# Kernel tuning notes

Measured on AMD Instinct MI355X. Metric: run time of the kernel, lower is better.

Reference implementation:

```python
import jax, jax.numpy as jnp
import numpy as np
import math

B, C, MAPS, HEADS, F, W = 2, 8, 4, 8, 256, 1024
HD = F // HEADS  # head dim = 32


def conv2d(x, w, b):
    # x [B,Ci,H,W], w [Co,Ci,3,3], SAME padding 1
    y = jax.lax.conv_general_dilated(x, w, (1, 1), [(1, 1), (1, 1)],
                                     dimension_numbers=('NCHW', 'OIHW', 'NCHW'))
    return y + b[None, :, None, None]


def mcl_feat(x, w):
    # MultichannelLinear feature transform: per-channel linear over feature dim
    # x [B,C,Fin,W], w [C,Fout,Fin] -> [B,C,Fout,W]
    return jnp.einsum('bcfw,cgf->bcgw', x, w)


def rope(x):
    # lucidrains-style rotary embedding over seq dim (-2); x [..., S, D]
    d = x.shape[-1]
    s = x.shape[-2]
    inv = 1.0 / (10000.0 ** (jnp.arange(0, d, 2, dtype=jnp.float32) / d))
    fr = jnp.arange(s, dtype=jnp.float32)[:, None] * inv[None, :]  # [S, D/2]
    cos = jnp.repeat(jnp.cos(fr), 2, axis=-1).astype(x.dtype)  # [S, D]
    sin = jnp.repeat(jnp.sin(fr), 2, axis=-1).astype(x.dtype)
    x2 = x.reshape(*x.shape[:-1], d // 2, 2)
    xr = jnp.stack((-x2[..., 1], x2[..., 0]), axis=-1).reshape(x.shape)
    return x * cos + xr * sin


def setup_inputs() -> dict:
    key = jax.random.key(0)
    ks = jax.random.split(key, 16)
    p = lambda k, shp, s=0.02: (jax.random.normal(k, shp, dtype=jnp.float32) * s)
    inp = {
        'x': jax.random.normal(ks[0], (B, C, F, W), dtype=jnp.float32),
        'prev_qk': jax.random.normal(ks[1], (B, MAPS, HEADS, W, W), dtype=jnp.float32),
        'wq_conv': p(ks[2], (MAPS, C, 3, 3)), 'bq_conv': jnp.zeros((MAPS,), jnp.float32),
        'wq_lin': p(ks[3], (MAPS, F, F)),
        'wk_conv': p(ks[4], (MAPS, C, 3, 3)), 'bk_conv': jnp.zeros((MAPS,), jnp.float32),
        'wk_lin': p(ks[5], (MAPS, F, F)),
        'wv_conv': p(ks[6], (MAPS, C, 3, 3)), 'bv_conv': jnp.zeros((MAPS,), jnp.float32),
        'wv_lin': p(ks[7], (MAPS, F, F)),
        'wo_pw': p(ks[8], (C + MAPS, F, F)),
        'wo_dw': p(ks[9], (C, C + MAPS)),
    }
    return inp


def reference(x, prev_qk, wq_conv, bq_conv, wq_lin, wk_conv, bk_conv, wk_lin,
              wv_conv, bv_conv, wv_lin, wo_pw, wo_dw):
    b, c, h, w = x.shape

    def proj(w_conv, b_conv, w_lin):
        y = mcl_feat(conv2d(x, w_conv, b_conv), w_lin)  # [B,M,F,W]
        # transpose(2,3) -> [B,M,W,F] -> split heads -> [B,M,Hd,W? ] permute
        y = y.transpose(0, 1, 3, 2).reshape(b, MAPS, w, HEADS, HD)
        return y.transpose(0, 1, 3, 2, 4)  # [B,M,Heads,W,HD]

    q = rope(proj(wq_conv, bq_conv, wq_lin))
    k = rope(proj(wk_conv, bk_conv, wk_lin))
    v = proj(wv_conv, bv_conv, wv_lin)

    # NOTE: scale is sqrt(h) = sqrt(feature/height dim), as in the original code
    qk = jnp.einsum('bmnqd,bmnkd->bmnqk', q, k) / math.sqrt(h)
    qk = qk + prev_qk
    a = jnp.einsum('bmnqk,bmnkd->bmnqd', jax.nn.softmax(qk, axis=-1), v)
    # [B,M,Heads,W,HD] -> [B,M,W,Heads*HD] -> [B,M,F,W]
    a = a.transpose(0, 1, 3, 2, 4).reshape(b, MAPS, w, -1).transpose(0, 1, 3, 2)

    cat = jnp.concatenate((x, a), axis=1)  # [B, C+M, F, W]
    out = jnp.einsum('bcfw,oc->bofw', mcl_feat(cat, wo_pw), wo_dw)  # o_proj
    return out, qk
```

## Files before the change

kernel.cpp:

```cpp
#include <hip/hip_runtime.h>
#include <hip/hip_bf16.h>
#include <stdint.h>


typedef __attribute__((ext_vector_type(8))) short s16x8;
typedef __attribute__((ext_vector_type(4))) float f32x4;

#define MFMA16(a, b, c) __builtin_amdgcn_mfma_f32_16x16x32_bf16((a), (b), (c), 0, 0, 0)

__device__ __forceinline__ short f2bf(float f) {
  unsigned u = __builtin_bit_cast(unsigned, f);
  u = (u + 0x7FFFu + ((u >> 16) & 1u)) >> 16;
  return (short)u;
}
__device__ __forceinline__ unsigned pack2(float a, float b) {
  return (unsigned)(unsigned short)f2bf(a) | ((unsigned)(unsigned short)f2bf(b) << 16);
}
__device__ __forceinline__ float bf2f(unsigned u) {
  return __builtin_bit_cast(float, u << 16);
}

__global__ __launch_bounds__(256) void k_prep(const float* wq, const float* wk,
                                              const float* wv, const float* wo,
                                              short* wlin, short* wob, float* ct, float* st) {
  int i = blockIdx.x * 256 + threadIdx.x;
  if (i < 262144) wlin[i] = f2bf(wq[i]);
  else if (i < 524288) wlin[i] = f2bf(wk[i - 262144]);
  else if (i < 786432) wlin[i] = f2bf(wv[i - 524288]);
  if (i < 786432) wob[i] = f2bf(wo[i]);
  if (i < 16384) {
    int w = i >> 4, j = i & 15;
    float inv = exp2f(-(float)j * (13.287712379549449f / 16.0f));
    float ang = (float)w * inv;
    ct[i] = cosf(ang);
    st[i] = sinf(ang);
  }
}

__device__ __forceinline__ void loadrow(float* r, const float* xc, int f, int w0) {
  if (f < 0 || f > 255) {
#pragma unroll
    for (int jj = 0; jj < 6; ++jj) r[jj] = 0.f;
    return;
  }
  const float* row = xc + f * 1024;
#pragma unroll
  for (int jj = 0; jj < 6; ++jj) {
    int wc = w0 - 1 + jj;
    r[jj] = (wc >= 0 && wc < 1024) ? row[wc] : 0.f;
  }
}

__global__ __launch_bounds__(256) void k_conv(const float* x, const float* wqc, const float* bq,
                                              const float* wkc, const float* bk,
                                              const float* wvc, const float* bv, short* y) {
  int blk = blockIdx.x;
  int m_ = blk >> 7;
  int b_ = (blk >> 6) & 1;
  int fs = blk & 63;
  int f0 = fs * 4;
  int w0 = threadIdx.x * 4;
  const float* xb = x + (size_t)b_ * 2097152;
  const float* wp_[3] = {wqc + m_ * 72, wkc + m_ * 72, wvc + m_ * 72};
  float bias_[3] = {bq[m_], bk[m_], bv[m_]};

  float acc[3][4][4];
#pragma unroll
  for (int p = 0; p < 3; ++p)
#pragma unroll
    for (int fi = 0; fi < 4; ++fi)
#pragma unroll
      for (int j = 0; j < 4; ++j) acc[p][fi][j] = bias_[p];

  for (int c = 0; c < 8; ++c) {
    const float* xc = xb + c * 262144;
    float w9[3][9];
#pragma unroll
    for (int p = 0; p < 3; ++p)
#pragma unroll
      for (int t = 0; t < 9; ++t) w9[p][t] = wp_[p][c * 9 + t];
    float rows[6][6];
#pragma unroll
    for (int ri = 0; ri < 6; ++ri) loadrow(rows[ri], xc, f0 - 1 + ri, w0);
#pragma unroll
    for (int fi = 0; fi < 4; ++fi) {
#pragma unroll
      for (int p = 0; p < 3; ++p) {
#pragma unroll
        for (int j = 0; j < 4; ++j) {
          float s = acc[p][fi][j];
          s += rows[fi][j] * w9[p][0] + rows[fi][j + 1] * w9[p][1] + rows[fi][j + 2] * w9[p][2];
          s += rows[fi + 1][j] * w9[p][3] + rows[fi + 1][j + 1] * w9[p][4] + rows[fi + 1][j + 2] * w9[p][5];
          s += rows[fi + 2][j] * w9[p][6] + rows[fi + 2][j + 1] * w9[p][7] + rows[fi + 2][j + 2] * w9[p][8];
          acc[p][fi][j] = s;
        }
      }
    }
  }
#pragma unroll
  for (int p = 0; p < 3; ++p) {
    int mat = p * 8 + b_ * 4 + m_;
    short* yp = y + (size_t)mat * 262144;
#pragma unroll
    for (int fi = 0; fi < 4; ++fi) {
      uint2 pk;
      pk.x = pack2(acc[p][fi][0], acc[p][fi][1]);
      pk.y = pack2(acc[p][fi][2], acc[p][fi][3]);
      *(uint2*)(yp + (f0 + fi) * 1024 + w0) = pk;
    }
  }
}

__global__ __launch_bounds__(256) void k_ty(const short* y, short* yT) {
  __shared__ short tile[64][66];
  int blk = blockIdx.x;
  int mat = blk >> 6;
  int t = blk & 63;
  int f0 = (t >> 4) * 64, w0 = (t & 15) * 64;
  int j = threadIdx.x & 63, i0 = threadIdx.x >> 6;
  const short* sp = y + (size_t)mat * 262144 + f0 * 1024 + w0;
#pragma unroll
  for (int k = 0; k < 16; ++k) {
    int i = i0 + k * 4;
    tile[j][i] = sp[i * 1024 + j];
  }
  __syncthreads();
  short* dp = yT + (size_t)mat * 262144 + w0 * 256 + f0;
#pragma unroll
  for (int k = 0; k < 16; ++k) {
    int i = i0 + k * 4;
    dp[i * 256 + j] = tile[i][j];
  }
}

__global__ __launch_bounds__(256) void k_tx(const float* x, short* xT) {
  __shared__ short tile[64][66];
  int blk = blockIdx.x;
  int mat = blk >> 6;
  int t = blk & 63;
  int f0 = (t >> 4) * 64, w0 = (t & 15) * 64;
  int j = threadIdx.x & 63, i0 = threadIdx.x >> 6;
  const float* sp = x + (size_t)mat * 262144 + f0 * 1024 + w0;
#pragma unroll
  for (int k = 0; k < 16; ++k) {
    int i = i0 + k * 4;
    tile[j][i] = f2bf(sp[i * 1024 + j]);
  }
  __syncthreads();
  short* dp = xT + (size_t)mat * 262144 + w0 * 256 + f0;
#pragma unroll
  for (int k = 0; k < 16; ++k) {
    int i = i0 + k * 4;
    dp[i * 256 + j] = tile[i][j];
  }
}

__global__ __launch_bounds__(256) void k_qkv(const short* wlin, const short* yT,
                                             const float* ct, const float* st,
                                             short* qws, short* kws, short* vws) {
  int blk = blockIdx.x;
  int pbm = blk >> 4, wt = blk & 15;
  int p = pbm >> 3, bm = pbm & 7;
  int m_ = bm & 3;
  int tid = threadIdx.x, wv = tid >> 6, l = tid & 63, lr = l & 15, lg = l >> 4;
  const short* wl = wlin + (p * 4 + m_) * 65536;
  const short* yp = yT + (size_t)pbm * 262144;
  int w0 = wt * 64;
  int G0 = wv * 64;
  f32x4 acc[4][4];
#pragma unroll
  for (int i = 0; i < 4; ++i)
#pragma unroll
    for (int j = 0; j < 4; ++j) acc[i][j] = (f32x4){0.f, 0.f, 0.f, 0.f};

  if (p < 2) {
    for (int kc = 0; kc < 256; kc += 32) {
      s16x8 A[4], Bf[4];
#pragma unroll
      for (int gs = 0; gs < 4; ++gs)
        A[gs] = *(const s16x8*)(wl + (G0 + gs * 16 + lr) * 256 + kc + lg * 8);
#pragma unroll
      for (int s = 0; s < 4; ++s)
        Bf[s] = *(const s16x8*)(yp + (w0 + s * 16 + lr) * 256 + kc + lg * 8);
#pragma unroll
      for (int gs = 0; gs < 4; ++gs)
#pragma unroll
        for (int s = 0; s < 4; ++s) acc[gs][s] = MFMA16(A[gs], Bf[s], acc[gs][s]);
    }
    short* dst = (p == 0) ? qws : kws;
    float scale = (p == 0) ? 0.0625f : 1.0f;
#pragma unroll
    for (int gs = 0; gs < 4; ++gs) {
      int g0v = G0 + gs * 16 + lg * 4;
      int h = g0v >> 5, d0 = g0v & 31;
      int i0 = d0 >> 1;
#pragma unroll
      for (int s = 0; s < 4; ++s) {
        int w = w0 + s * 16 + lr;
        float c0 = ct[w * 16 + i0], sn0 = st[w * 16 + i0];
        float c1 = ct[w * 16 + i0 + 1], sn1 = st[w * 16 + i0 + 1];
        f32x4 v = acc[gs][s];
        float e0 = (v[0] * c0 - v[1] * sn0) * scale;
        float e1 = (v[1] * c0 + v[0] * sn0) * scale;
        float e2 = (v[2] * c1 - v[3] * sn1) * scale;
        float e3 = (v[3] * c1 + v[2] * sn1) * scale;
        uint2 pk;
        pk.x = pack2(e0, e1);
        pk.y = pack2(e2, e3);
        *(uint2*)(dst + (((size_t)bm * 8 + h) * 1024 + w) * 32 + d0) = pk;
      }
    }
  } else {
    for (int kc = 0; kc < 256; kc += 32) {
      s16x8 A[4], Bf[4];
#pragma unroll
      for (int s = 0; s < 4; ++s)
        A[s] = *(const s16x8*)(yp + (w0 + s * 16 + lr) * 256 + kc + lg * 8);
#pragma unroll
      for (int gs = 0; gs < 4; ++gs)
        Bf[gs] = *(const s16x8*)(wl + (G0 + gs * 16 + lr) * 256 + kc + lg * 8);
#pragma unroll
      for (int s = 0; s < 4; ++s)
#pragma unroll
        for (int gs = 0; gs < 4; ++gs) acc[s][gs] = MFMA16(A[s], Bf[gs], acc[s][gs]);
    }
#pragma unroll
    for (int s = 0; s < 4; ++s) {
      int wb = w0 + s * 16 + lg * 4;
#pragma unroll
      for (int gs = 0; gs < 4; ++gs) {
        int g = G0 + gs * 16 + lr;
        f32x4 v = acc[s][gs];
        uint2 pk;
        pk.x = pack2(v[0], v[1]);
        pk.y = pack2(v[2], v[3]);
        *(uint2*)(vws + ((size_t)bm * 256 + g) * 1024 + wb) = pk;
      }
    }
  }
}

__device__ __forceinline__ void attn_tile(int t, int tn, f32x4 (&pc)[4], f32x4 (&pn)[4],
                                          const float* pptr, float* qoptr,
                                          const short* kp, const short* vp,
                                          const s16x8& qf, char* Sb, char* Pb,
                                          int lr, int lg, f32x4& o0, f32x4& o1, f32x4& ps) {
#pragma unroll
  for (int j = 0; j < 4; ++j)
    pn[j] = *(const f32x4*)(pptr + j * 4096 + tn * 64);
  int k0 = t * 64;
  s16x8 kf[4];
#pragma unroll
  for (int s = 0; s < 4; ++s)
    kf[s] = *(const s16x8*)(kp + (k0 + s * 16 + lr) * 32 + lg * 8);
  const f32x4 z4 = {0.f, 0.f, 0.f, 0.f};
#pragma unroll
  for (int s = 0; s < 4; ++s) {
    f32x4 Sx = MFMA16(kf[s], qf, z4);
    *(f32x4*)(Sb + lr * 256 + ((s * 64 + lg * 16) ^ ((lr & 7) << 4))) = Sx;
  }
#pragma unroll
  for (int j = 0; j < 4; ++j) {
    int r = j * 4 + lg;
    f32x4 rv = *(const f32x4*)(Sb + r * 256 + ((lr * 16) ^ ((r & 7) << 4)));
    rv += pc[j];
    __builtin_nontemporal_store(rv, (f32x4*)(qoptr + j * 4096 + t * 64));
    float e0 = __expf(rv[0]), e1 = __expf(rv[1]);
    float e2 = __expf(rv[2]), e3 = __expf(rv[3]);
    ps[j] += (e0 + e1) + (e2 + e3);
    uint2 pk;
    pk.x = pack2(e0, e1);
    pk.y = pack2(e2, e3);
    *(uint2*)(Pb + r * 128 + ((lr * 8) ^ ((r & 7) << 4))) = pk;
  }
#pragma unroll
  for (int kc = 0; kc < 2; ++kc) {
    s16x8 pa = *(const s16x8*)(Pb + lr * 128 + ((kc * 64 + lg * 16) ^ ((lr & 7) << 4)));
    s16x8 vf0 = *(const s16x8*)(vp + lr * 1024 + k0 + kc * 32 + lg * 8);
    o0 = MFMA16(pa, vf0, o0);
    s16x8 vf1 = *(const s16x8*)(vp + (16 + lr) * 1024 + k0 + kc * 32 + lg * 8);
    o1 = MFMA16(pa, vf1, o1);
  }
}

__global__ __launch_bounds__(256, 4) void k_attn(const short* qws, const short* kws,
                                                 const short* vws, const float* prev,
                                                 float* qko, short* aT) {
  int blk = blockIdx.x;
  int bmh = blk >> 4;
  int h = bmh & 7;
  int bm = bmh >> 3;
  int tid = threadIdx.x;
  int wv = tid >> 6, l = tid & 63, lr = l & 15, lg = l >> 4;
  int qt = (blk & 15) * 4 + wv;
  int q0 = qt * 16;
  const short* qp = qws + (size_t)bmh * 32768;
  const short* kp = kws + (size_t)bmh * 32768;
  const short* vp = vws + ((size_t)bm * 256 + h * 32) * 1024;
  const float* pptr = prev + (size_t)bmh * 1048576 + (size_t)(q0 + lg) * 1024 + lr * 4;
  float* qoptr = qko + (size_t)bmh * 1048576 + (size_t)(q0 + lg) * 1024 + lr * 4;

  __shared__ float s_s[4][16][64];
  __shared__ short s_p[4][16][64];
  char* Sb = (char*)&s_s[wv][0][0];
  char* Pb = (char*)&s_p[wv][0][0];

  s16x8 qf = *(const s16x8*)(qp + (q0 + lr) * 32 + lg * 8);
  f32x4 o0 = {0.f, 0.f, 0.f, 0.f}, o1 = {0.f, 0.f, 0.f, 0.f};
  f32x4 ps = {0.f, 0.f, 0.f, 0.f};

  f32x4 pA[4], pB[4];
#pragma unroll
  for (int j = 0; j < 4; ++j) pA[j] = *(const f32x4*)(pptr + j * 4096);

  for (int t = 0; t < 16; t += 2) {
    attn_tile(t, t + 1, pA, pB, pptr, qoptr, kp, vp, qf, Sb, Pb, lr, lg, o0, o1, ps);
    attn_tile(t + 1, (t + 2 < 16) ? t + 2 : 15, pB, pA, pptr, qoptr, kp, vp, qf, Sb, Pb, lr, lg, o0, o1, ps);
  }

#pragma unroll
  for (int j = 0; j < 4; ++j) {
    float s = ps[j];
    s += __shfl_xor(s, 1);
    s += __shfl_xor(s, 2);
    s += __shfl_xor(s, 4);
    s += __shfl_xor(s, 8);
    ps[j] = s;
  }
  if (lr == 0) {
#pragma unroll
    for (int j = 0; j < 4; ++j) *(float*)(Sb + (j * 4 + lg) * 4) = ps[j];
  }
  f32x4 sums = *(const f32x4*)(Sb + lg * 16);
  f32x4 inv = {1.f / sums[0], 1.f / sums[1], 1.f / sums[2], 1.f / sums[3]};
  o0 *= inv;
  o1 *= inv;
  short* ap = aT + (size_t)bm * 262144;
#pragma unroll
  for (int r = 0; r < 4; ++r) {
    int row = q0 + lg * 4 + r;
    ap[row * 256 + h * 32 + lr] = f2bf(o0[r]);
    ap[row * 256 + h * 32 + 16 + lr] = f2bf(o1[r]);
  }
}

__global__ __launch_bounds__(256) void k_zproj(const short* wopw, const short* xT,
                                               const short* aT, short* z) {
  int blk = blockIdx.x;
  int bc = blk >> 4, wt = blk & 15;
  int b_ = bc / 12, c_ = bc % 12;
  const short* src = (c_ < 8) ? (xT + ((size_t)b_ * 8 + c_) * 262144)
                              : (aT + ((size_t)b_ * 4 + (c_ - 8)) * 262144);
  const short* wl = wopw + c_ * 65536;
  int tid = threadIdx.x, wv = tid >> 6, l = tid & 63, lr = l & 15, lg = l >> 4;
  int w0 = wt * 64, G0 = wv * 64;
  f32x4 acc[4][4];
#pragma unroll
  for (int i = 0; i < 4; ++i)
#pragma unroll
    for (int j = 0; j < 4; ++j) acc[i][j] = (f32x4){0.f, 0.f, 0.f, 0.f};
  for (int kc = 0; kc < 256; kc += 32) {
    s16x8 A[4], Bf[4];
#pragma unroll
    for (int s = 0; s < 4; ++s)
      A[s] = *(const s16x8*)(src + (w0 + s * 16 + lr) * 256 + kc + lg * 8);
#pragma unroll
    for (int gs = 0; gs < 4; ++gs)
      Bf[gs] = *(const s16x8*)(wl + (G0 + gs * 16 + lr) * 256 + kc + lg * 8);
#pragma unroll
    for (int s = 0; s < 4; ++s)
#pragma unroll
      for (int gs = 0; gs < 4; ++gs) acc[s][gs] = MFMA16(A[s], Bf[gs], acc[s][gs]);
  }
  short* zp = z + (size_t)bc * 262144;
#pragma unroll
  for (int s = 0; s < 4; ++s) {
    int wb = w0 + s * 16 + lg * 4;
#pragma unroll
    for (int gs = 0; gs < 4; ++gs) {
      int g = G0 + gs * 16 + lr;
      f32x4 v = acc[s][gs];
      uint2 pk;
      pk.x = pack2(v[0], v[1]);
      pk.y = pack2(v[2], v[3]);
      *(uint2*)(zp + g * 1024 + wb) = pk;
    }
  }
}

__global__ __launch_bounds__(256) void k_dw(const short* z, const float* dw, float* out0) {
  __shared__ float wdw[96];
  if (threadIdx.x < 96) wdw[threadIdx.x] = dw[threadIdx.x];
  __syncthreads();
  int id = blockIdx.x * 256 + threadIdx.x;
  int w4 = id & 255, g = (id >> 8) & 255, b_ = id >> 16;
  const short* zb = z + ((size_t)b_ * 12) * 262144 + g * 1024 + w4 * 4;
  float zv[12][4];
#pragma unroll
  for (int c = 0; c < 12; ++c) {
    uint2 u = *(const uint2*)(zb + (size_t)c * 262144);
    zv[c][0] = bf2f(u.x & 0xffffu);
    zv[c][1] = bf2f(u.x >> 16);
    zv[c][2] = bf2f(u.y & 0xffffu);
    zv[c][3] = bf2f(u.y >> 16);
  }
  float* ob = out0 + ((size_t)b_ * 8) * 262144 + g * 1024 + w4 * 4;
#pragma unroll
  for (int o = 0; o < 8; ++o) {
    f32x4 s = {0.f, 0.f, 0.f, 0.f};
#pragma unroll
    for (int c = 0; c < 12; ++c) {
      float wc = wdw[o * 12 + c];
      s[0] += wc * zv[c][0];
      s[1] += wc * zv[c][1];
      s[2] += wc * zv[c][2];
      s[3] += wc * zv[c][3];
    }
    __builtin_nontemporal_store(s, (f32x4*)(ob + (size_t)o * 262144));
  }
}

extern "C" void kernel_launch(void* const* d_in, const int* in_sizes, int n_in,
                              void* d_out, int out_size, void* d_ws, size_t ws_size,
                              hipStream_t stream) {
  const float* x = (const float*)d_in[0];
  const float* prevqk = (const float*)d_in[1];
  const float* wq_conv = (const float*)d_in[2];
  const float* bq = (const float*)d_in[3];
  const float* wq_lin = (const float*)d_in[4];
  const float* wk_conv = (const float*)d_in[5];
  const float* bk = (const float*)d_in[6];
  const float* wk_lin = (const float*)d_in[7];
  const float* wv_conv = (const float*)d_in[8];
  const float* bv = (const float*)d_in[9];
  const float* wv_lin = (const float*)d_in[10];
  const float* wo_pw = (const float*)d_in[11];
  const float* wo_dw = (const float*)d_in[12];

  float* out0 = (float*)d_out;
  float* qkout = out0 + 4194304;

  char* ws = (char*)d_ws;
  short* wlin_b = (short*)ws;
  short* wopw_b = wlin_b + 786432;
  float* ct = (float*)(ws + 3145728);
  float* st = ct + 16384;
  short* y_b = (short*)(ws + 3276800);
  short* yT_b = y_b + 6291456;
  short* q_b = yT_b + 6291456;
  short* k_b = q_b + 2097152;
  short* v_b = k_b + 2097152;
  short* xT_b = v_b + 2097152;
  short* aT_b = xT_b + 4194304;
  short* z_b = (short*)(ws + 53608448);

  k_prep<<<3072, 256, 0, stream>>>(wq_lin, wk_lin, wv_lin, wo_pw, wlin_b, wopw_b, ct, st);
  k_conv<<<512, 256, 0, stream>>>(x, wq_conv, bq, wk_conv, bk, wv_conv, bv, y_b);
  k_ty<<<1536, 256, 0, stream>>>(y_b, yT_b);
  k_tx<<<1024, 256, 0, stream>>>(x, xT_b);
  k_qkv<<<384, 256, 0, stream>>>(wlin_b, yT_b, ct, st, q_b, k_b, v_b);
  k_attn<<<1024, 256, 0, stream>>>(q_b, k_b, v_b, prevqk, qkout, aT_b);
  k_zproj<<<384, 256, 0, stream>>>(wopw_b, xT_b, aT_b, z_b);
  k_dw<<<512, 256, 0, stream>>>(z_b, wo_dw, out0);
}
```

Measured before the change: 241.6 us.

## Restructure attention into single-wave blocks with 256-key windows and row-contiguous prev_qk access

Each block of the attention kernel becomes a single 64-lane wave that owns 16 query rows, and keys are processed in 256-wide windows. The score tile is staged through 16KB of shared memory so each lane reads and writes contiguous 16-byte chunks along a full 1024-float row of prev_qk and the qk output, instead of the earlier 64-float strips. This is meant to improve coalescing of the dominant fp32 prev_qk read and qk write, and to issue 16 row loads per window for more memory-level parallelism. In exchange it uses more registers and shared memory per wave, gives up the previous double-buffered prefetch, and adds a shared-memory reduction for the row sums.

```diff
diff --git a/kernel.cpp b/kernel.cpp
--- a/kernel.cpp
+++ b/kernel.cpp
@@ -240,98 +240,91 @@
   }
 }
 
-__device__ __forceinline__ void attn_tile(int t, int tn, f32x4 (&pc)[4], f32x4 (&pn)[4],
-                                          const float* pptr, float* qoptr,
-                                          const short* kp, const short* vp,
-                                          const s16x8& qf, char* Sb, char* Pb,
-                                          int lr, int lg, f32x4& o0, f32x4& o1, f32x4& ps) {
-#pragma unroll
-  for (int j = 0; j < 4; ++j)
-    pn[j] = *(const f32x4*)(pptr + j * 4096 + tn * 64);
-  int k0 = t * 64;
-  s16x8 kf[4];
-#pragma unroll
-  for (int s = 0; s < 4; ++s)
-    kf[s] = *(const s16x8*)(kp + (k0 + s * 16 + lr) * 32 + lg * 8);
-  const f32x4 z4 = {0.f, 0.f, 0.f, 0.f};
-#pragma unroll
-  for (int s = 0; s < 4; ++s) {
-    f32x4 Sx = MFMA16(kf[s], qf, z4);
-    *(f32x4*)(Sb + lr * 256 + ((s * 64 + lg * 16) ^ ((lr & 7) << 4))) = Sx;
-  }
-#pragma unroll
-  for (int j = 0; j < 4; ++j) {
-    int r = j * 4 + lg;
-    f32x4 rv = *(const f32x4*)(Sb + r * 256 + ((lr * 16) ^ ((r & 7) << 4)));
-    rv += pc[j];
-    __builtin_nontemporal_store(rv, (f32x4*)(qoptr + j * 4096 + t * 64));
-    float e0 = __expf(rv[0]), e1 = __expf(rv[1]);
-    float e2 = __expf(rv[2]), e3 = __expf(rv[3]);
-    ps[j] += (e0 + e1) + (e2 + e3);
-    uint2 pk;
-    pk.x = pack2(e0, e1);
-    pk.y = pack2(e2, e3);
-    *(uint2*)(Pb + r * 128 + ((lr * 8) ^ ((r & 7) << 4))) = pk;
-  }
-#pragma unroll
-  for (int kc = 0; kc < 2; ++kc) {
-    s16x8 pa = *(const s16x8*)(Pb + lr * 128 + ((kc * 64 + lg * 16) ^ ((lr & 7) << 4)));
-    s16x8 vf0 = *(const s16x8*)(vp + lr * 1024 + k0 + kc * 32 + lg * 8);
-    o0 = MFMA16(pa, vf0, o0);
-    s16x8 vf1 = *(const s16x8*)(vp + (16 + lr) * 1024 + k0 + kc * 32 + lg * 8);
-    o1 = MFMA16(pa, vf1, o1);
-  }
-}
-
-__global__ __launch_bounds__(256, 4) void k_attn(const short* qws, const short* kws,
-                                                 const short* vws, const float* prev,
-                                                 float* qko, short* aT) {
-  int blk = blockIdx.x;
-  int bmh = blk >> 4;
+__global__ __launch_bounds__(64, 2) void k_attn(const short* qws, const short* kws,
+                                                const short* vws, const float* prev,
+                                                float* qko, short* aT) {
+  int blk = blockIdx.x;
+  int bmh = blk >> 6;
+  int qt = blk & 63;
   int h = bmh & 7;
   int bm = bmh >> 3;
-  int tid = threadIdx.x;
-  int wv = tid >> 6, l = tid & 63, lr = l & 15, lg = l >> 4;
-  int qt = (blk & 15) * 4 + wv;
+  int l = threadIdx.x;
+  int lr = l & 15, lg = l >> 4;
   int q0 = qt * 16;
   const short* qp = qws + (size_t)bmh * 32768;
   const short* kp = kws + (size_t)bmh * 32768;
   const short* vp = vws + ((size_t)bm * 256 + h * 32) * 1024;
-  const float* pptr = prev + (size_t)bmh * 1048576 + (size_t)(q0 + lg) * 1024 + lr * 4;
-  float* qoptr = qko + (size_t)bmh * 1048576 + (size_t)(q0 + lg) * 1024 + lr * 4;
-
-  __shared__ float s_s[4][16][64];
-  __shared__ short s_p[4][16][64];
-  char* Sb = (char*)&s_s[wv][0][0];
-  char* Pb = (char*)&s_p[wv][0][0];
+  const float* pvb = prev + (size_t)bmh * 1048576 + (size_t)q0 * 1024 + l * 4;
+  float* qob = qko + (size_t)bmh * 1048576 + (size_t)q0 * 1024 + l * 4;
+
+  __shared__ char smem[16384];
+  int swl = (l & 7) << 4;
 
   s16x8 qf = *(const s16x8*)(qp + (q0 + lr) * 32 + lg * 8);
   f32x4 o0 = {0.f, 0.f, 0.f, 0.f}, o1 = {0.f, 0.f, 0.f, 0.f};
-  f32x4 ps = {0.f, 0.f, 0.f, 0.f};
-
-  f32x4 pA[4], pB[4];
-#pragma unroll
-  for (int j = 0; j < 4; ++j) pA[j] = *(const f32x4*)(pptr + j * 4096);
-
-  for (int t = 0; t < 16; t += 2) {
-    attn_tile(t, t + 1, pA, pB, pptr, qoptr, kp, vp, qf, Sb, Pb, lr, lg, o0, o1, ps);
-    attn_tile(t + 1, (t + 2 < 16) ? t + 2 : 15, pB, pA, pptr, qoptr, kp, vp, qf, Sb, Pb, lr, lg, o0, o1, ps);
-  }
-
-#pragma unroll
-  for (int j = 0; j < 4; ++j) {
-    float s = ps[j];
-    s += __shfl_xor(s, 1);
-    s += __shfl_xor(s, 2);
-    s += __shfl_xor(s, 4);
-    s += __shfl_xor(s, 8);
-    ps[j] = s;
-  }
-  if (lr == 0) {
-#pragma unroll
-    for (int j = 0; j < 4; ++j) *(float*)(Sb + (j * 4 + lg) * 4) = ps[j];
-  }
-  f32x4 sums = *(const f32x4*)(Sb + lg * 16);
+  float rs[16];
+#pragma unroll
+  for (int r = 0; r < 16; ++r) rs[r] = 0.f;
+  const f32x4 z4 = {0.f, 0.f, 0.f, 0.f};
+  int swlr = (lr & 7) << 4;
+
+  for (int win = 0; win < 4; ++win) {
+    int kw = win * 256;
+    f32x4 pr[16];
+#pragma unroll
+    for (int r = 0; r < 16; ++r) pr[r] = *(const f32x4*)(pvb + (size_t)r * 1024 + kw);
+
+#pragma unroll
+    for (int t = 0; t < 4; ++t) {
+      s16x8 kf[4];
+#pragma unroll
+      for (int s = 0; s < 4; ++s)
+        kf[s] = *(const s16x8*)(kp + (kw + t * 64 + s * 16 + lr) * 32 + lg * 8);
+#pragma unroll
+      for (int s = 0; s < 4; ++s) {
+        f32x4 Sx = MFMA16(kf[s], qf, z4);
+        *(f32x4*)(smem + lr * 1024 + ((t * 256 + s * 64 + lg * 16) ^ swlr)) = Sx;
+      }
+    }
+
+#pragma unroll
+    for (int r = 0; r < 16; ++r) {
+      f32x4 sv = *(const f32x4*)(smem + r * 1024 + ((l * 16) ^ ((r & 7) << 4)));
+      f32x4 v = sv + pr[r];
+      __builtin_nontemporal_store(v, (f32x4*)(qob + (size_t)r * 1024 + kw));
+      float e0 = __expf(v[0]), e1 = __expf(v[1]);
+      float e2 = __expf(v[2]), e3 = __expf(v[3]);
+      rs[r] += (e0 + e1) + (e2 + e3);
+      uint2 pk;
+      pk.x = pack2(e0, e1);
+      pk.y = pack2(e2, e3);
+      *(uint2*)(smem + r * 512 + ((l * 8) ^ ((r & 7) << 4))) = pk;
+    }
+
+#pragma unroll
+    for (int t = 0; t < 4; ++t) {
+#pragma unroll
+      for (int kc = 0; kc < 2; ++kc) {
+        s16x8 pa = *(const s16x8*)(smem + lr * 512 + ((t * 128 + kc * 64 + lg * 16) ^ swlr));
+        s16x8 vf0 = *(const s16x8*)(vp + lr * 1024 + kw + t * 64 + kc * 32 + lg * 8);
+        o0 = MFMA16(pa, vf0, o0);
+        s16x8 vf1 = *(const s16x8*)(vp + (16 + lr) * 1024 + kw + t * 64 + kc * 32 + lg * 8);
+        o1 = MFMA16(pa, vf1, o1);
+      }
+    }
+  }
+
+  float* sred = (float*)smem;
+#pragma unroll
+  for (int r = 0; r < 16; ++r) sred[r * 64 + l] = rs[r];
+  int rj = l >> 2, c0 = (l & 3) * 16;
+  float tsum = 0.f;
+#pragma unroll
+  for (int j = 0; j < 16; ++j) tsum += sred[rj * 64 + c0 + j];
+  tsum += __shfl_xor(tsum, 1);
+  tsum += __shfl_xor(tsum, 2);
+  if ((l & 3) == 0) *(float*)(smem + 8192 + rj * 4) = tsum;
+  f32x4 sums = *(const f32x4*)(smem + 8192 + lg * 16);
   f32x4 inv = {1.f / sums[0], 1.f / sums[1], 1.f / sums[2], 1.f / sums[3]};
   o0 *= inv;
   o1 *= inv;
@@ -459,7 +452,7 @@
   k_ty<<<1536, 256, 0, stream>>>(y_b, yT_b);
   k_tx<<<1024, 256, 0, stream>>>(x, xT_b);
   k_qkv<<<384, 256, 0, stream>>>(wlin_b, yT_b, ct, st, q_b, k_b, v_b);
-  k_attn<<<1024, 256, 0, stream>>>(q_b, k_b, v_b, prevqk, qkout, aT_b);
+  k_attn<<<4096, 64, 0, stream>>>(q_b, k_b, v_b, prevqk, qkout, aT_b);
   k_zproj<<<384, 256, 0, stream>>>(wopw_b, xT_b, aT_b, z_b);
   k_dw<<<512, 256, 0, stream>>>(z_b, wo_dw, out0);
 }
```

New measurement: 243.3 us. Within noise of the previous version (+0.7%).

## Stage full K and V for a head in LDS and deepen prev_qk prefetch

Applied to the files above, without the earlier changes.

The attention kernel now copies the whole K (1024x32) and V (32x1024) slice for its head into a large swizzled shared-memory buffer once per block, then reads K and V fragments from LDS instead of global memory. The prev_qk prefetch is moved two windows ahead, issued after the P stores. The aim is to cut repeated global or L2 traffic for K/V and hide prev_qk latency. The ~152KB of LDS and launch_bounds(256,1) limit occupancy to one block per CU, which reduces latency hiding on what is mostly a memory-bound stream of prev_qk and qk.

```diff
diff --git a/kernel.cpp b/kernel.cpp
--- a/kernel.cpp
+++ b/kernel.cpp
@@ -240,96 +240,114 @@
   }
 }
 
-__device__ __forceinline__ void attn_tile(int t, int tn, f32x4 (&pc)[4], f32x4 (&pn)[4],
-                                          const float* pptr, float* qoptr,
-                                          const short* kp, const short* vp,
-                                          const s16x8& qf, char* Sb, char* Pb,
-                                          int lr, int lg, f32x4& o0, f32x4& o1, f32x4& ps) {
-#pragma unroll
-  for (int j = 0; j < 4; ++j)
-    pn[j] = *(const f32x4*)(pptr + j * 4096 + tn * 64);
-  int k0 = t * 64;
-  s16x8 kf[4];
-#pragma unroll
-  for (int s = 0; s < 4; ++s)
-    kf[s] = *(const s16x8*)(kp + (k0 + s * 16 + lr) * 32 + lg * 8);
-  const f32x4 z4 = {0.f, 0.f, 0.f, 0.f};
-#pragma unroll
-  for (int s = 0; s < 4; ++s) {
-    f32x4 Sx = MFMA16(kf[s], qf, z4);
-    *(f32x4*)(Sb + lr * 256 + ((s * 64 + lg * 16) ^ ((lr & 7) << 4))) = Sx;
-  }
-#pragma unroll
-  for (int j = 0; j < 4; ++j) {
-    int r = j * 4 + lg;
-    f32x4 rv = *(const f32x4*)(Sb + r * 256 + ((lr * 16) ^ ((r & 7) << 4)));
-    rv += pc[j];
-    __builtin_nontemporal_store(rv, (f32x4*)(qoptr + j * 4096 + t * 64));
-    float e0 = __expf(rv[0]), e1 = __expf(rv[1]);
-    float e2 = __expf(rv[2]), e3 = __expf(rv[3]);
-    ps[j] += (e0 + e1) + (e2 + e3);
-    uint2 pk;
-    pk.x = pack2(e0, e1);
-    pk.y = pack2(e2, e3);
-    *(uint2*)(Pb + r * 128 + ((lr * 8) ^ ((r & 7) << 4))) = pk;
-  }
-#pragma unroll
-  for (int kc = 0; kc < 2; ++kc) {
-    s16x8 pa = *(const s16x8*)(Pb + lr * 128 + ((kc * 64 + lg * 16) ^ ((lr & 7) << 4)));
-    s16x8 vf0 = *(const s16x8*)(vp + lr * 1024 + k0 + kc * 32 + lg * 8);
-    o0 = MFMA16(pa, vf0, o0);
-    s16x8 vf1 = *(const s16x8*)(vp + (16 + lr) * 1024 + k0 + kc * 32 + lg * 8);
-    o1 = MFMA16(pa, vf1, o1);
-  }
-}
-
-__global__ __launch_bounds__(256, 4) void k_attn(const short* qws, const short* kws,
+__global__ __launch_bounds__(256, 1) void k_attn(const short* qws, const short* kws,
                                                  const short* vws, const float* prev,
                                                  float* qko, short* aT) {
+  __shared__ char smem[155648];
   int blk = blockIdx.x;
   int bmh = blk >> 4;
-  int h = bmh & 7;
-  int bm = bmh >> 3;
+  int qg = blk & 15;
+  int h = bmh & 7, bm = bmh >> 3;
   int tid = threadIdx.x;
   int wv = tid >> 6, l = tid & 63, lr = l & 15, lg = l >> 4;
-  int qt = (blk & 15) * 4 + wv;
-  int q0 = qt * 16;
-  const short* qp = qws + (size_t)bmh * 32768;
   const short* kp = kws + (size_t)bmh * 32768;
   const short* vp = vws + ((size_t)bm * 256 + h * 32) * 1024;
-  const float* pptr = prev + (size_t)bmh * 1048576 + (size_t)(q0 + lg) * 1024 + lr * 4;
-  float* qoptr = qko + (size_t)bmh * 1048576 + (size_t)(q0 + lg) * 1024 + lr * 4;
-
-  __shared__ float s_s[4][16][64];
-  __shared__ short s_p[4][16][64];
-  char* Sb = (char*)&s_s[wv][0][0];
-  char* Pb = (char*)&s_p[wv][0][0];
-
+
+  {
+    int row4 = tid >> 2, c = tid & 3;
+#pragma unroll
+    for (int i = 0; i < 16; ++i) {
+      int row = i * 64 + row4;
+      s16x8 kv = *(const s16x8*)(kp + row * 32 + c * 8);
+      *(s16x8*)(smem + row * 64 + ((c * 16) ^ ((row & 3) << 4))) = kv;
+    }
+    int g2 = tid >> 7, cb = (tid & 127) * 16;
+#pragma unroll
+    for (int i = 0; i < 16; ++i) {
+      int g = i * 2 + g2;
+      s16x8 vv = *(const s16x8*)(vp + g * 1024 + (cb >> 1));
+      *(s16x8*)(smem + 65536 + g * 2048 + (cb ^ ((g & 7) << 4))) = vv;
+    }
+  }
+  __syncthreads();
+
+  int q0 = qg * 64 + wv * 16;
+  const short* qp = qws + (size_t)bmh * 32768;
   s16x8 qf = *(const s16x8*)(qp + (q0 + lr) * 32 + lg * 8);
+  char* Sb = smem + 131072 + wv * 4096;
+  char* Pb = smem + 147456 + wv * 2048;
+  const float* pvb = prev + (size_t)bmh * 1048576 + (size_t)q0 * 1024;
+  float* qob = qko + (size_t)bmh * 1048576 + (size_t)q0 * 1024;
+  int pcol = (l & 15) * 4;
+  int pcolb = pcol * 4;
   f32x4 o0 = {0.f, 0.f, 0.f, 0.f}, o1 = {0.f, 0.f, 0.f, 0.f};
-  f32x4 ps = {0.f, 0.f, 0.f, 0.f};
+  f32x4 rs = {0.f, 0.f, 0.f, 0.f};
+  const f32x4 z4 = {0.f, 0.f, 0.f, 0.f};
+
+  auto attn_win = [&](int w, f32x4(&pr)[4]) {
+    int k0 = w * 64;
+#pragma unroll
+    for (int s = 0; s < 4; ++s) {
+      int krow = k0 + s * 16 + lr;
+      s16x8 kf = *(const s16x8*)(smem + krow * 64 + ((lg * 16) ^ ((krow & 3) << 4)));
+      f32x4 sx = MFMA16(kf, qf, z4);
+      *(f32x4*)(Sb + lr * 256 + ((s * 64 + lg * 16) ^ ((lr & 7) << 4))) = sx;
+    }
+#pragma unroll
+    for (int j = 0; j < 4; ++j) {
+      int qr = j * 4 + lg;
+      f32x4 sv = *(const f32x4*)(Sb + qr * 256 + (pcolb ^ ((qr & 7) << 4)));
+      f32x4 v = sv + pr[j];
+      __builtin_nontemporal_store(v, (f32x4*)(qob + (size_t)qr * 1024 + k0 + pcol));
+      float e0 = __expf(v[0]), e1 = __expf(v[1]);
+      float e2 = __expf(v[2]), e3 = __expf(v[3]);
+      rs[j] += (e0 + e1) + (e2 + e3);
+      uint2 pk;
+      pk.x = pack2(e0, e1);
+      pk.y = pack2(e2, e3);
+      *(uint2*)(Pb + qr * 128 + (((l & 15) * 8) ^ ((qr & 7) << 4))) = pk;
+    }
+    if (w + 2 < 16) {
+#pragma unroll
+      for (int j = 0; j < 4; ++j)
+        pr[j] = *(const f32x4*)(pvb + (size_t)(j * 4 + lg) * 1024 + (w + 2) * 64 + pcol);
+    }
+#pragma unroll
+    for (int kc = 0; kc < 2; ++kc) {
+      s16x8 pa = *(const s16x8*)(Pb + lr * 128 + ((kc * 64 + lg * 16) ^ ((lr & 7) << 4)));
+      int kcb = (k0 + kc * 32 + lg * 8) * 2;
+      s16x8 vf0 = *(const s16x8*)(smem + 65536 + lr * 2048 + (kcb ^ ((lr & 7) << 4)));
+      o0 = MFMA16(pa, vf0, o0);
+      s16x8 vf1 = *(const s16x8*)(smem + 65536 + (16 + lr) * 2048 + (kcb ^ ((lr & 7) << 4)));
+      o1 = MFMA16(pa, vf1, o1);
+    }
+  };
 
   f32x4 pA[4], pB[4];
 #pragma unroll
-  for (int j = 0; j < 4; ++j) pA[j] = *(const f32x4*)(pptr + j * 4096);
-
-  for (int t = 0; t < 16; t += 2) {
-    attn_tile(t, t + 1, pA, pB, pptr, qoptr, kp, vp, qf, Sb, Pb, lr, lg, o0, o1, ps);
-    attn_tile(t + 1, (t + 2 < 16) ? t + 2 : 15, pB, pA, pptr, qoptr, kp, vp, qf, Sb, Pb, lr, lg, o0, o1, ps);
+  for (int j = 0; j < 4; ++j)
+    pA[j] = *(const f32x4*)(pvb + (size_t)(j * 4 + lg) * 1024 + 0 + pcol);
+#pragma unroll
+  for (int j = 0; j < 4; ++j)
+    pB[j] = *(const f32x4*)(pvb + (size_t)(j * 4 + lg) * 1024 + 64 + pcol);
+
+  for (int w = 0; w < 16; w += 2) {
+    attn_win(w, pA);
+    attn_win(w + 1, pB);
   }
 
 #pragma unroll
   for (int j = 0; j < 4; ++j) {
-    float s = ps[j];
+    float s = rs[j];
     s += __shfl_xor(s, 1);
     s += __shfl_xor(s, 2);
     s += __shfl_xor(s, 4);
     s += __shfl_xor(s, 8);
-    ps[j] = s;
+    rs[j] = s;
   }
   if (lr == 0) {
 #pragma unroll
-    for (int j = 0; j < 4; ++j) *(float*)(Sb + (j * 4 + lg) * 4) = ps[j];
+    for (int j = 0; j < 4; ++j) *(float*)(Sb + (j * 4 + lg) * 4) = rs[j];
   }
   f32x4 sums = *(const f32x4*)(Sb + lg * 16);
   f32x4 inv = {1.f / sums[0], 1.f / sums[1], 1.f / sums[2], 1.f / sums[3]};
```

New measurement: 232.6 us. 1.04x faster.

## Restructure attention to stage full bf16 score rows in LDS with row-wise softmax

Applied to the files above, without the earlier changes.

The attention kernel now runs in three phases instead of interleaving per 64-key tile. First it computes all QK scores for a wave's 16 queries into a 32KB bf16 LDS buffer. It then does a row-by-row pass that reads prev_qk and writes qk over whole contiguous 1024-float rows, prefetching three rows ahead and overwriting the scores with exp values. Finally it runs the PV MFMAs. The goal is fully coalesced streaming of the large prev/qk tensors. The cost is 128KB of shared memory per block, which limits occupancy to one block per CU, and the scores are rounded to bf16 before prev_qk is added.

```diff
diff --git a/kernel.cpp b/kernel.cpp
--- a/kernel.cpp
+++ b/kernel.cpp
@@ -240,101 +240,113 @@
   }
 }
 
-__device__ __forceinline__ void attn_tile(int t, int tn, f32x4 (&pc)[4], f32x4 (&pn)[4],
-                                          const float* pptr, float* qoptr,
-                                          const short* kp, const short* vp,
-                                          const s16x8& qf, char* Sb, char* Pb,
-                                          int lr, int lg, f32x4& o0, f32x4& o1, f32x4& ps) {
-#pragma unroll
-  for (int j = 0; j < 4; ++j)
-    pn[j] = *(const f32x4*)(pptr + j * 4096 + tn * 64);
-  int k0 = t * 64;
-  s16x8 kf[4];
-#pragma unroll
-  for (int s = 0; s < 4; ++s)
-    kf[s] = *(const s16x8*)(kp + (k0 + s * 16 + lr) * 32 + lg * 8);
-  const f32x4 z4 = {0.f, 0.f, 0.f, 0.f};
-#pragma unroll
-  for (int s = 0; s < 4; ++s) {
-    f32x4 Sx = MFMA16(kf[s], qf, z4);
-    *(f32x4*)(Sb + lr * 256 + ((s * 64 + lg * 16) ^ ((lr & 7) << 4))) = Sx;
-  }
-#pragma unroll
-  for (int j = 0; j < 4; ++j) {
-    int r = j * 4 + lg;
-    f32x4 rv = *(const f32x4*)(Sb + r * 256 + ((lr * 16) ^ ((r & 7) << 4)));
-    rv += pc[j];
-    __builtin_nontemporal_store(rv, (f32x4*)(qoptr + j * 4096 + t * 64));
-    float e0 = __expf(rv[0]), e1 = __expf(rv[1]);
-    float e2 = __expf(rv[2]), e3 = __expf(rv[3]);
-    ps[j] += (e0 + e1) + (e2 + e3);
-    uint2 pk;
-    pk.x = pack2(e0, e1);
-    pk.y = pack2(e2, e3);
-    *(uint2*)(Pb + r * 128 + ((lr * 8) ^ ((r & 7) << 4))) = pk;
-  }
-#pragma unroll
-  for (int kc = 0; kc < 2; ++kc) {
-    s16x8 pa = *(const s16x8*)(Pb + lr * 128 + ((kc * 64 + lg * 16) ^ ((lr & 7) << 4)));
-    s16x8 vf0 = *(const s16x8*)(vp + lr * 1024 + k0 + kc * 32 + lg * 8);
-    o0 = MFMA16(pa, vf0, o0);
-    s16x8 vf1 = *(const s16x8*)(vp + (16 + lr) * 1024 + k0 + kc * 32 + lg * 8);
-    o1 = MFMA16(pa, vf1, o1);
-  }
-}
-
-__global__ __launch_bounds__(256, 4) void k_attn(const short* qws, const short* kws,
+__global__ __launch_bounds__(256, 1) void k_attn(const short* qws, const short* kws,
                                                  const short* vws, const float* prev,
                                                  float* qko, short* aT) {
+  __shared__ char smem[131072];
   int blk = blockIdx.x;
   int bmh = blk >> 4;
-  int h = bmh & 7;
-  int bm = bmh >> 3;
+  int qg = blk & 15;
+  int h = bmh & 7, bm = bmh >> 3;
   int tid = threadIdx.x;
   int wv = tid >> 6, l = tid & 63, lr = l & 15, lg = l >> 4;
-  int qt = (blk & 15) * 4 + wv;
-  int q0 = qt * 16;
+  int q0 = qg * 64 + wv * 16;
   const short* qp = qws + (size_t)bmh * 32768;
   const short* kp = kws + (size_t)bmh * 32768;
   const short* vp = vws + ((size_t)bm * 256 + h * 32) * 1024;
-  const float* pptr = prev + (size_t)bmh * 1048576 + (size_t)(q0 + lg) * 1024 + lr * 4;
-  float* qoptr = qko + (size_t)bmh * 1048576 + (size_t)(q0 + lg) * 1024 + lr * 4;
-
-  __shared__ float s_s[4][16][64];
-  __shared__ short s_p[4][16][64];
-  char* Sb = (char*)&s_s[wv][0][0];
-  char* Pb = (char*)&s_p[wv][0][0];
+  const float* pvb = prev + (size_t)bmh * 1048576 + (size_t)q0 * 1024;
+  float* qob = qko + (size_t)bmh * 1048576 + (size_t)q0 * 1024;
+  char* Sb = smem + wv * 32768;
 
   s16x8 qf = *(const s16x8*)(qp + (q0 + lr) * 32 + lg * 8);
-  f32x4 o0 = {0.f, 0.f, 0.f, 0.f}, o1 = {0.f, 0.f, 0.f, 0.f};
-  f32x4 ps = {0.f, 0.f, 0.f, 0.f};
-
-  f32x4 pA[4], pB[4];
-#pragma unroll
-  for (int j = 0; j < 4; ++j) pA[j] = *(const f32x4*)(pptr + j * 4096);
-
-  for (int t = 0; t < 16; t += 2) {
-    attn_tile(t, t + 1, pA, pB, pptr, qoptr, kp, vp, qf, Sb, Pb, lr, lg, o0, o1, ps);
-    attn_tile(t + 1, (t + 2 < 16) ? t + 2 : 15, pB, pA, pptr, qoptr, kp, vp, qf, Sb, Pb, lr, lg, o0, o1, ps);
-  }
-
-#pragma unroll
-  for (int j = 0; j < 4; ++j) {
-    float s = ps[j];
+  const f32x4 z4 = {0.f, 0.f, 0.f, 0.f};
+
+#pragma unroll
+  for (int w = 0; w < 16; ++w) {
+    int k0 = w * 64;
+    s16x8 kf[4];
+#pragma unroll
+    for (int s = 0; s < 4; ++s)
+      kf[s] = *(const s16x8*)(kp + (k0 + s * 16 + lr) * 32 + lg * 8);
+#pragma unroll
+    for (int s = 0; s < 4; ++s) {
+      f32x4 sx = MFMA16(kf[s], qf, z4);
+      uint2 pk;
+      pk.x = pack2(sx[0], sx[1]);
+      pk.y = pack2(sx[2], sx[3]);
+      int kb = (k0 + s * 16 + lg * 4) * 2;
+      *(uint2*)(Sb + lr * 2048 + (kb ^ ((lr & 7) << 4))) = pk;
+    }
+  }
+
+  float rs[16];
+  f32x4 pf[3][4];
+#pragma unroll
+  for (int qt = 0; qt < 4; ++qt) pf[0][qt] = *(const f32x4*)(pvb + 0 * 1024 + qt * 256 + l * 4);
+#pragma unroll
+  for (int qt = 0; qt < 4; ++qt) pf[1][qt] = *(const f32x4*)(pvb + 1 * 1024 + qt * 256 + l * 4);
+#pragma unroll
+  for (int qt = 0; qt < 4; ++qt) pf[2][qt] = *(const f32x4*)(pvb + 2 * 1024 + qt * 256 + l * 4);
+
+#pragma unroll
+  for (int r = 0; r < 16; ++r) {
+    float sum = 0.f;
+#pragma unroll
+    for (int qt = 0; qt < 4; ++qt) {
+      int sb = (qt * 512 + l * 8) ^ ((r & 7) << 4);
+      uint2 su = *(const uint2*)(Sb + r * 2048 + sb);
+      f32x4 sv = {bf2f(su.x & 0xffffu), bf2f(su.x >> 16),
+                  bf2f(su.y & 0xffffu), bf2f(su.y >> 16)};
+      f32x4 v = sv + pf[r % 3][qt];
+      *(f32x4*)(qob + (size_t)r * 1024 + qt * 256 + l * 4) = v;
+      float e0 = __expf(v[0]), e1 = __expf(v[1]);
+      float e2 = __expf(v[2]), e3 = __expf(v[3]);
+      sum += (e0 + e1) + (e2 + e3);
+      uint2 pk;
+      pk.x = pack2(e0, e1);
+      pk.y = pack2(e2, e3);
+      *(uint2*)(Sb + r * 2048 + sb) = pk;
+    }
+    if (r + 3 < 16) {
+#pragma unroll
+      for (int qt = 0; qt < 4; ++qt)
+        pf[r % 3][qt] = *(const f32x4*)(pvb + (size_t)(r + 3) * 1024 + qt * 256 + l * 4);
+    }
+    rs[r] = sum;
+  }
+#pragma unroll
+  for (int r = 0; r < 16; ++r) {
+    float s = rs[r];
     s += __shfl_xor(s, 1);
     s += __shfl_xor(s, 2);
     s += __shfl_xor(s, 4);
     s += __shfl_xor(s, 8);
-    ps[j] = s;
-  }
-  if (lr == 0) {
-#pragma unroll
-    for (int j = 0; j < 4; ++j) *(float*)(Sb + (j * 4 + lg) * 4) = ps[j];
-  }
-  f32x4 sums = *(const f32x4*)(Sb + lg * 16);
-  f32x4 inv = {1.f / sums[0], 1.f / sums[1], 1.f / sums[2], 1.f / sums[3]};
-  o0 *= inv;
-  o1 *= inv;
+    s += __shfl_xor(s, 16);
+    s += __shfl_xor(s, 32);
+    rs[r] = s;
+  }
+
+  f32x4 o0 = {0.f, 0.f, 0.f, 0.f}, o1 = {0.f, 0.f, 0.f, 0.f};
+#pragma unroll
+  for (int w = 0; w < 16; ++w) {
+    int k0 = w * 64;
+#pragma unroll
+    for (int kc = 0; kc < 2; ++kc) {
+      int kb = (k0 + kc * 32 + lg * 8) * 2;
+      s16x8 pa = *(const s16x8*)(Sb + lr * 2048 + (kb ^ ((lr & 7) << 4)));
+      s16x8 vf0 = *(const s16x8*)(vp + lr * 1024 + k0 + kc * 32 + lg * 8);
+      o0 = MFMA16(pa, vf0, o0);
+      s16x8 vf1 = *(const s16x8*)(vp + (16 + lr) * 1024 + k0 + kc * 32 + lg * 8);
+      o1 = MFMA16(pa, vf1, o1);
+    }
+  }
+#pragma unroll
+  for (int j = 0; j < 4; ++j) {
+    float s = (lg == 0) ? rs[j] : (lg == 1) ? rs[4 + j] : (lg == 2) ? rs[8 + j] : rs[12 + j];
+    float inv = 1.0f / s;
+    o0[j] *= inv;
+    o1[j] *= inv;
+  }
   short* ap = aT + (size_t)bm * 262144;
 #pragma unroll
   for (int r = 0; r < 4; ++r) {
```

Result: slower. 253.2 us (+4.8%).
